# Optimization experiments

Measured on AMD Instinct MI355X. Metric: run time of the kernel, lower is better.

The kernel has to match this reference:

```python
import jax, jax.numpy as jnp
import numpy as np

B, T, D, H = 512, 256, 64, 128


def _uniform(key, shape, stdv):
    return jax.random.uniform(key, shape, jnp.float32, -stdv, stdv)


def setup_inputs() -> dict:
    key = jax.random.key(0)
    ks = jax.random.split(key, 20)
    x_t = jax.random.normal(ks[0], (B, T, D), jnp.float32)
    masks = (jax.random.uniform(ks[1], (B, T, D)) < 0.8).astype(jnp.float32)
    deltas = jax.random.uniform(ks[2], (B, T, D), jnp.float32)
    sH = 1.0 / np.sqrt(H)
    sD = 1.0 / np.sqrt(D)
    return {
        "x_t": x_t, "masks": masks, "deltas": deltas,
        # TemporalDecay h: [H, D]
        "Wdh": _uniform(ks[3], (H, D), sH), "bdh": _uniform(ks[4], (H,), sH),
        # TemporalDecay x (diag): [D, D]
        "Wdx": _uniform(ks[5], (D, D), sD), "bdx": _uniform(ks[6], (D,), sD),
        # hist_reg Linear(H -> D)
        "Whr": _uniform(ks[7], (D, H), sH), "bhr": _uniform(ks[8], (D,), sH),
        "Wfr": _uniform(ks[9], (D, D), sD), "bfr": _uniform(ks[10], (D,), sD),
        # weight_combine Linear(2D -> D)
        "Wwc": _uniform(ks[11], (D, 2 * D), 1.0 / np.sqrt(2 * D)),
        "bwc": _uniform(ks[12], (D,), 1.0 / np.sqrt(2 * D)),
        # LSTMCell(2D -> H)
        "W_ih": _uniform(ks[13], (4 * H, 2 * D), sH), "W_hh": _uniform(ks[14], (4 * H, H), sH),
        "b_ih": _uniform(ks[15], (4 * H,), sH), "b_hh": _uniform(ks[16], (4 * H,), sH),
    }


def reference(x_t, masks, deltas, Wdh, bdh, Wdx, bdx, Whr, bhr, Wfr, bfr, Wwc, bwc, W_ih, W_hh, b_ih, b_hh):
    Bv, Tv, Dv = x_t.shape
    Hv = Wdh.shape[0]
    eye = jnp.eye(Dv, dtype=x_t.dtype)
    Wdx_m = Wdx * eye              # diagonal temporal decay
    Wfr_m = Wfr * (1.0 - eye)

    def step(carry, xs):
        h, c, loss = carry
        x, m, d = xs
        gamma_h = jnp.exp(-jax.nn.relu(d @ Wdh.T + bdh))   # [B,H]
        gamma_x = jnp.exp(-jax.nn.relu(d @ Wdx_m.T + bdx))  # [B,D]
        h = h * gamma_h
        x_h = h @ Whr.T + bhr
        msum = jnp.sum(m) + 1e-5
        loss = loss + jnp.sum(jnp.abs(x - x_h) * m) / msum
        x_c = m * x + (1.0 - m) * x_h
        z_h = x_c @ Wfr_m.T + bfr
        loss = loss + jnp.sum(jnp.abs(x - z_h) * m) / msum
        alpha = jnp.concatenate([gamma_x, m], axis=1) @ Wwc.T + bwc
        c_h = alpha * z_h + (1.0 - alpha) * x_h
        loss = loss + jnp.sum(jnp.abs(x - c_h) * m) / msum
        c_c = m * x + (1.0 - m) * c_h
        inp = jnp.concatenate([c_c, m], axis=1)            # [B,2D]
        gates = inp @ W_ih.T + b_ih + h @ W_hh.T + b_hh    # [B,4H]
        i, f, g, o = jnp.split(gates, 4, axis=1)
        c = jax.nn.sigmoid(f) * c + jax.nn.sigmoid(i) * jnp.tanh(g)
        h = jax.nn.sigmoid(o) * jnp.tanh(c)
        return (h, c, loss), c_c

    h0 = jnp.zeros((Bv, Hv), x_t.dtype)
    c0 = jnp.zeros((Bv, Hv), x_t.dtype)
    xs = (jnp.swapaxes(x_t, 0, 1), jnp.swapaxes(masks, 0, 1), jnp.swapaxes(deltas, 0, 1))
    (h, c, loss), imps = jax.lax.scan(step, (h0, c0, jnp.float32(0.0)), xs)
    imputations = jnp.swapaxes(imps, 0, 1)                 # [B,T,D]
    return loss / Tv, imputations
```

## Files before the change

### kernel.cpp

```cpp
#include <hip/hip_runtime.h>
#include <hip/hip_bf16.h>

typedef __bf16 bf16x8 __attribute__((ext_vector_type(8)));
typedef float f32x4 __attribute__((ext_vector_type(4)));

#define NB 512
#define NT 256
#define ND 64
#define NH 128
#define PART_IDX 256
#define FLAG_IDX 320

__device__ __forceinline__ float bf2f(__hip_bfloat16 v){ return __bfloat162float(v); }
__device__ __forceinline__ __hip_bfloat16 f2bf(float v){ return __float2bfloat16(v); }

__device__ __forceinline__ float ldF(const float* p){ return *p; }
__device__ __forceinline__ float ldF(const __hip_bfloat16* p){ return __bfloat162float(*p); }
__device__ __forceinline__ void  stF(float* p, float v){ *p = v; }
__device__ __forceinline__ void  stF(__hip_bfloat16* p, float v){ *p = __float2bfloat16(v); }

__device__ __forceinline__ void ld2(const float* p, float& a, float& b){
    float2 v = *reinterpret_cast<const float2*>(p); a = v.x; b = v.y;
}
__device__ __forceinline__ void ld2(const __hip_bfloat16* p, float& a, float& b){
    unsigned u = *reinterpret_cast<const unsigned*>(p);
    unsigned short s0 = (unsigned short)(u & 0xffffu), s1 = (unsigned short)(u >> 16);
    a = __bfloat162float(*reinterpret_cast<__hip_bfloat16*>(&s0));
    b = __bfloat162float(*reinterpret_cast<__hip_bfloat16*>(&s1));
}

__device__ __forceinline__ bf16x8 ldfrag(const __hip_bfloat16* p){
    return *reinterpret_cast<const bf16x8*>(p);
}
__device__ __forceinline__ bf16x8 ldfrag(const float* p){
    f32x4 a = *reinterpret_cast<const f32x4*>(p);
    f32x4 b = *reinterpret_cast<const f32x4*>(p + 4);
    bf16x8 r;
    #pragma unroll
    for (int i = 0; i < 4; ++i){
        __hip_bfloat16 ha = __float2bfloat16(a[i]);
        __hip_bfloat16 hb = __float2bfloat16(b[i]);
        r[i]   = *reinterpret_cast<__bf16*>(&ha);
        r[4+i] = *reinterpret_cast<__bf16*>(&hb);
    }
    return r;
}
__device__ __forceinline__ bf16x8 ldbf8(const __hip_bfloat16* p){
    return *reinterpret_cast<const bf16x8*>(p);
}

template<typename T> __device__ __forceinline__ float wantFlag(){ return sizeof(T)==4 ? 1.f : 0.f; }

__device__ __forceinline__ f32x4 mfma16(bf16x8 a, bf16x8 b, f32x4 c){
    return __builtin_amdgcn_mfma_f32_16x16x32_bf16(a, b, c, 0, 0, 0);
}
__device__ __forceinline__ float fsig(float x){ return 1.f/(1.f+__expf(-x)); }
__device__ __forceinline__ float ftanh(float x){ return 1.f - 2.f/(__expf(2.f*x)+1.f); }

__global__ void detect_kernel(const void* __restrict__ x, float* __restrict__ WS){
    if (threadIdx.x == 0 && blockIdx.x == 0){
        const unsigned short* u = (const unsigned short*)x;
        int weird = 0;
        for (int i = 0; i < 256; ++i){
            unsigned e = (u[i] >> 7) & 0xFF;
            if (e == 0xFF || e >= 0x8A || (e != 0 && e <= 0x5A)) ++weird;
        }
        WS[FLAG_IDX] = (weird >= 16) ? 1.f : 0.f;
    }
}

template<typename T>
__global__ __launch_bounds__(256) void msum_kernel(const T* __restrict__ M,
                                                   float* __restrict__ WS){
    if (WS[FLAG_IDX] != wantFlag<T>()) return;
    int t = blockIdx.x;
    int tid = threadIdx.x;
    int col = tid & 63;
    int bg  = tid >> 6;
    float s = 0.f;
    for (int b = bg; b < NB; b += 4)
        s += ldF(&M[((size_t)b*NT + t)*ND + col]);
    #pragma unroll
    for (int off = 32; off > 0; off >>= 1) s += __shfl_down(s, off);
    __shared__ float r4[4];
    if ((tid & 63) == 0) r4[bg] = s;
    __syncthreads();
    if (tid == 0) WS[t] = 1.f / (r4[0] + r4[1] + r4[2] + r4[3] + 1e-5f);
}

template<typename T>
__global__ __launch_bounds__(512, 2) void brits_main(
    const T* __restrict__ X,  const T* __restrict__ M,
    const T* __restrict__ DL,
    const T* __restrict__ Wdh, const T* __restrict__ bdh,
    const T* __restrict__ Wdx, const T* __restrict__ bdx,
    const T* __restrict__ Whr, const T* __restrict__ bhr,
    const T* __restrict__ Wfr, const T* __restrict__ bfr,
    const T* __restrict__ Wwc, const T* __restrict__ bwc,
    const T* __restrict__ Wih, const T* __restrict__ Whh,
    const T* __restrict__ bih, const T* __restrict__ bhh,
    T* __restrict__ OUT, float* __restrict__ WS)
{
    if (WS[FLAG_IDX] != wantFlag<T>()) return;

    __shared__ __align__(16) __hip_bfloat16 sAg[16][264];
    __shared__ __align__(16) __hip_bfloat16 sAal[16][136];
    __shared__ __align__(16) __hip_bfloat16 sXc[16][72];
    __shared__ __align__(16) __hip_bfloat16 sDL[16][72];
    __shared__ float sX [16][68];
    __shared__ float sXh[16][68];
    __shared__ float sZh[16][68];
    __shared__ float sAl[16][68];
    __shared__ float sRed[8];

    const int tid = threadIdx.x;
    const int w  = tid >> 6;
    const int l  = tid & 63;
    const int lr = l & 15;
    const int lg = l >> 4;
    const int b0 = blockIdx.x * 16;

    const int hcol = 16*w + lr;
    const float bdh_r = ldF(&bdh[hcol]);
    const float gb_i = ldF(&bih[hcol])      + ldF(&bhh[hcol]);
    const float gb_f = ldF(&bih[NH+hcol])   + ldF(&bhh[NH+hcol]);
    const float gb_g = ldF(&bih[2*NH+hcol]) + ldF(&bhh[2*NH+hcol]);
    const float gb_o = ldF(&bih[3*NH+hcol]) + ldF(&bhh[3*NH+hcol]);

    bf16x8 pB0 = ldfrag(Wdh + (size_t)hcol*ND + lg*8);
    bf16x8 pB1 = ldfrag(Wdh + (size_t)hcol*ND + 32 + lg*8);
    bf16x8 qB0 = {}, qB1 = {}, qB2 = {}, qB3 = {}, rB0 = {}, rB1 = {};
    float b1_r = 0.f, b2_r = 0.f, b3_r = 0.f;
    int dcol;
    if (w < 4){
        dcol = 16*w + lr;
        b1_r = ldF(&bhr[dcol]);  b2_r = ldF(&bfr[dcol]);
        qB0 = ldfrag(Whr + (size_t)dcol*NH + lg*8);
        qB1 = ldfrag(Whr + (size_t)dcol*NH + 32 + lg*8);
        qB2 = ldfrag(Whr + (size_t)dcol*NH + 64 + lg*8);
        qB3 = ldfrag(Whr + (size_t)dcol*NH + 96 + lg*8);
        rB0 = ldfrag(Wfr + (size_t)dcol*ND + lg*8);
        rB1 = ldfrag(Wfr + (size_t)dcol*ND + 32 + lg*8);
        int kb0 = lg*8;      if (dcol >= kb0 && dcol < kb0+8) rB0[dcol-kb0] = (__bf16)0.f;
        int kb1 = 32 + lg*8; if (dcol >= kb1 && dcol < kb1+8) rB1[dcol-kb1] = (__bf16)0.f;
    } else {
        dcol = 16*(w-4) + lr;
        b3_r = ldF(&bwc[dcol]);
        qB0 = ldfrag(Wwc + (size_t)dcol*2*ND + lg*8);
        qB1 = ldfrag(Wwc + (size_t)dcol*2*ND + 32 + lg*8);
        qB2 = ldfrag(Wwc + (size_t)dcol*2*ND + 64 + lg*8);
        qB3 = ldfrag(Wwc + (size_t)dcol*2*ND + 96 + lg*8);
    }

    const int r0 = tid >> 5;
    const int c0 = (tid & 31) * 2;
    const float wdg0 = ldF(&Wdx[(size_t)c0*ND + c0]);
    const float wdg1 = ldF(&Wdx[(size_t)(c0+1)*ND + (c0+1)]);
    const float bdx0 = ldF(&bdx[c0]);
    const float bdx1 = ldF(&bdx[c0+1]);

    float hreg[4] = {0.f,0.f,0.f,0.f};
    float creg[4] = {0.f,0.f,0.f,0.f};
    float lacc = 0.f;

    float pd0, pd1, pm0, pm1, px0, px1;

    {
        size_t g0 = ((size_t)(b0+r0)*NT + 0)*ND + c0;
        ld2(DL + g0, pd0, pd1);
        ld2(M  + g0, pm0, pm1);
        ld2(X  + g0, px0, px1);
        sDL[r0][c0]   = f2bf(pd0);
        sDL[r0][c0+1] = f2bf(pd1);
        #pragma unroll
        for (int r = 0; r < 4; ++r) sAg[lg*4+r][128 + hcol] = f2bf(0.f);
    }
    float inv_cur = WS[0];
    __syncthreads();

    #pragma unroll 1
    for (int t = 0; t < NT; ++t){
        const float inv_ms = inv_cur;
        {
            f32x4 acc = {0.f,0.f,0.f,0.f};
            acc = mfma16(ldbf8(&sDL[lr][0  + lg*8]), pB0, acc);
            acc = mfma16(ldbf8(&sDL[lr][32 + lg*8]), pB1, acc);
            #pragma unroll
            for (int r = 0; r < 4; ++r){
                float gm = __expf(-fmaxf(acc[r] + bdh_r, 0.f));
                hreg[r] *= gm;
                sAg[lg*4+r][128 + hcol] = f2bf(hreg[r]);
            }
            float gx0 = __expf(-fmaxf(pd0*wdg0 + bdx0, 0.f));
            float gx1 = __expf(-fmaxf(pd1*wdg1 + bdx1, 0.f));
            sAal[r0][c0]      = f2bf(gx0);
            sAal[r0][c0+1]    = f2bf(gx1);
            sAal[r0][64+c0]   = f2bf(pm0);
            sAal[r0][64+c0+1] = f2bf(pm1);
            sAg[r0][64+c0]    = f2bf(pm0);
            sAg[r0][64+c0+1]  = f2bf(pm1);
            sX[r0][c0]   = px0;
            sX[r0][c0+1] = px1;
        }
        __syncthreads();
        if (w < 4){
            f32x4 acc = {0.f,0.f,0.f,0.f};
            acc = mfma16(ldbf8(&sAg[lr][128 + 0  + lg*8]), qB0, acc);
            acc = mfma16(ldbf8(&sAg[lr][128 + 32 + lg*8]), qB1, acc);
            acc = mfma16(ldbf8(&sAg[lr][128 + 64 + lg*8]), qB2, acc);
            acc = mfma16(ldbf8(&sAg[lr][128 + 96 + lg*8]), qB3, acc);
            #pragma unroll
            for (int r = 0; r < 4; ++r){
                int row = lg*4 + r;
                float xh = acc[r] + b1_r;
                sXh[row][dcol] = xh;
                float mv = bf2f(sAg[row][64+dcol]);
                float xv = sX[row][dcol];
                float xc = mv*xv + (1.f-mv)*xh;
                sXc[row][dcol] = f2bf(xc);
                lacc += fabsf(xv - xh) * mv * inv_ms;
            }
        } else {
            f32x4 acc = {0.f,0.f,0.f,0.f};
            acc = mfma16(ldbf8(&sAal[lr][0  + lg*8]), qB0, acc);
            acc = mfma16(ldbf8(&sAal[lr][32 + lg*8]), qB1, acc);
            acc = mfma16(ldbf8(&sAal[lr][64 + lg*8]), qB2, acc);
            acc = mfma16(ldbf8(&sAal[lr][96 + lg*8]), qB3, acc);
            #pragma unroll
            for (int r = 0; r < 4; ++r) sAl[lg*4+r][dcol] = acc[r] + b3_r;
        }
        __syncthreads();
        if (w < 4){
            f32x4 acc = {0.f,0.f,0.f,0.f};
            acc = mfma16(ldbf8(&sXc[lr][0  + lg*8]), rB0, acc);
            acc = mfma16(ldbf8(&sXc[lr][32 + lg*8]), rB1, acc);
            #pragma unroll
            for (int r = 0; r < 4; ++r) sZh[lg*4+r][dcol] = acc[r] + b2_r;
        }
        __syncthreads();
        {
            size_t g = ((size_t)(b0+r0)*NT + t)*ND + c0;
            #pragma unroll
            for (int e = 0; e < 2; ++e){
                int col = c0 + e;
                float xv = sX[r0][col];
                float mv = bf2f(sAg[r0][64+col]);
                float zh = sZh[r0][col];
                float xh = sXh[r0][col];
                float al = sAl[r0][col];
                float ch = al*zh + (1.f-al)*xh;
                lacc += (fabsf(xv - zh) + fabsf(xv - ch)) * mv * inv_ms;
                float cc = mv*xv + (1.f-mv)*ch;
                stF(&OUT[1 + g + e], cc);
                sAg[r0][col] = f2bf(cc);
            }
        }
        __syncthreads();
        {
            const int tn = (t+1 < NT) ? t+1 : t;
            size_t gE = ((size_t)(b0+r0)*NT + tn)*ND + c0;
            ld2(DL + gE, pd0, pd1);
            ld2(M  + gE, pm0, pm1);
            ld2(X  + gE, px0, px1);
            float inv_next = WS[tn];

            bf16x8 af[8];
            #pragma unroll
            for (int kk = 0; kk < 8; ++kk) af[kk] = ldbf8(&sAg[lr][kk*32 + lg*8]);
            const T* wih_b = Wih + (size_t)hcol*128;
            const T* whh_b = Whh + (size_t)hcol*128;
            f32x4 gacc[4];
            #pragma unroll
            for (int g = 0; g < 4; ++g){
                const T* wr = wih_b + (size_t)g*NH*128;
                const T* hr = whh_b + (size_t)g*NH*128;
                f32x4 a = {0.f,0.f,0.f,0.f};
                a = mfma16(af[0], ldfrag(wr + 0  + lg*8), a);
                a = mfma16(af[1], ldfrag(wr + 32 + lg*8), a);
                a = mfma16(af[2], ldfrag(wr + 64 + lg*8), a);
                a = mfma16(af[3], ldfrag(wr + 96 + lg*8), a);
                a = mfma16(af[4], ldfrag(hr + 0  + lg*8), a);
                a = mfma16(af[5], ldfrag(hr + 32 + lg*8), a);
                a = mfma16(af[6], ldfrag(hr + 64 + lg*8), a);
                a = mfma16(af[7], ldfrag(hr + 96 + lg*8), a);
                gacc[g] = a;
            }
            #pragma unroll
            for (int r = 0; r < 4; ++r){
                float iv = fsig(gacc[0][r] + gb_i);
                float fv = fsig(gacc[1][r] + gb_f);
                float gv = ftanh(gacc[2][r] + gb_g);
                float ov = fsig(gacc[3][r] + gb_o);
                creg[r] = fv*creg[r] + iv*gv;
                hreg[r] = ov*ftanh(creg[r]);
            }
            sDL[r0][c0]   = f2bf(pd0);
            sDL[r0][c0+1] = f2bf(pd1);
            inv_cur = inv_next;
        }
        __syncthreads();
    }

    #pragma unroll
    for (int off = 32; off > 0; off >>= 1) lacc += __shfl_down(lacc, off);
    if (l == 0) sRed[w] = lacc;
    __syncthreads();
    if (tid == 0){
        float s = 0.f;
        #pragma unroll
        for (int i = 0; i < 8; ++i) s += sRed[i];
        WS[PART_IDX + blockIdx.x] = s;
    }
}

template<typename T>
__global__ void fin_kernel(const float* __restrict__ WS, T* __restrict__ OUT){
    if (WS[FLAG_IDX] != wantFlag<T>()) return;
    if (threadIdx.x == 0 && blockIdx.x == 0){
        float s = 0.f;
        for (int i = 0; i < 32; ++i) s += WS[PART_IDX + i];
        stF(&OUT[0], s / (float)NT);
    }
}

template<typename T>
static void launch_all(void* const* d_in, void* d_out, float* WS, hipStream_t stream){
    const T* X   = (const T*)d_in[0];
    const T* M   = (const T*)d_in[1];
    const T* DL  = (const T*)d_in[2];
    const T* Wdh = (const T*)d_in[3];
    const T* bdh = (const T*)d_in[4];
    const T* Wdx = (const T*)d_in[5];
    const T* bdx = (const T*)d_in[6];
    const T* Whr = (const T*)d_in[7];
    const T* bhr = (const T*)d_in[8];
    const T* Wfr = (const T*)d_in[9];
    const T* bfr = (const T*)d_in[10];
    const T* Wwc = (const T*)d_in[11];
    const T* bwc = (const T*)d_in[12];
    const T* Wih = (const T*)d_in[13];
    const T* Whh = (const T*)d_in[14];
    const T* bih = (const T*)d_in[15];
    const T* bhh = (const T*)d_in[16];
    T* OUT = (T*)d_out;
    msum_kernel<T><<<dim3(NT), dim3(256), 0, stream>>>(M, WS);
    brits_main<T><<<dim3(32), dim3(512), 0, stream>>>(X, M, DL, Wdh, bdh, Wdx, bdx,
                                                      Whr, bhr, Wfr, bfr, Wwc, bwc,
                                                      Wih, Whh, bih, bhh, OUT, WS);
    fin_kernel<T><<<dim3(1), dim3(64), 0, stream>>>(WS, OUT);
}

extern "C" void kernel_launch(void* const* d_in, const int* in_sizes, int n_in,
                              void* d_out, int out_size, void* d_ws, size_t ws_size,
                              hipStream_t stream) {
    float* WS = (float*)d_ws;
    detect_kernel<<<dim3(1), dim3(64), 0, stream>>>(d_in[0], WS);
    launch_all<__hip_bfloat16>(d_in, d_out, WS, stream);
    launch_all<float>(d_in, d_out, WS, stream);
}
```

Baseline: 805.3 us.

## Fold decay phase into LSTM phase and double-buffer h/mask to drop a barrier

Moves the gamma_h decay GEMM (loading deltas for the next step straight from global memory into MFMA fragments) and the gamma_x/mask/x staging into the tail of the previous step's LSTM phase. The separate first phase and its __syncthreads are removed from each timestep. h and mask are double-buffered in shared memory and the concatenated LSTM input buffer is split into separate arrays. This removes one barrier per step and shortens the serial chain, at the cost of extra global loads and MFMAs in the LSTM phase. It also stores only the decayed h rather than keeping h in registers.

```diff
diff --git a/kernel.cpp b/kernel.cpp
--- a/kernel.cpp
+++ b/kernel.cpp
@@ -48,6 +48,33 @@
 __device__ __forceinline__ bf16x8 ldbf8(const __hip_bfloat16* p){
     return *reinterpret_cast<const bf16x8*>(p);
 }
+
+template<typename T> struct PF;
+template<> struct PF<float>{
+    f32x4 a, b;
+    __device__ __forceinline__ void load(const float* p){
+        a = *reinterpret_cast<const f32x4*>(p);
+        b = *reinterpret_cast<const f32x4*>(p + 4);
+    }
+    __device__ __forceinline__ bf16x8 get() const {
+        bf16x8 r;
+        #pragma unroll
+        for (int i = 0; i < 4; ++i){
+            __hip_bfloat16 ha = __float2bfloat16(a[i]);
+            __hip_bfloat16 hb = __float2bfloat16(b[i]);
+            r[i]   = *reinterpret_cast<const __bf16*>(&ha);
+            r[4+i] = *reinterpret_cast<const __bf16*>(&hb);
+        }
+        return r;
+    }
+};
+template<> struct PF<__hip_bfloat16>{
+    bf16x8 a;
+    __device__ __forceinline__ void load(const __hip_bfloat16* p){
+        a = *reinterpret_cast<const bf16x8*>(p);
+    }
+    __device__ __forceinline__ bf16x8 get() const { return a; }
+};
 
 template<typename T> __device__ __forceinline__ float wantFlag(){ return sizeof(T)==4 ? 1.f : 0.f; }
 
@@ -103,10 +130,11 @@
 {
     if (WS[FLAG_IDX] != wantFlag<T>()) return;
 
-    __shared__ __align__(16) __hip_bfloat16 sAg[16][264];
-    __shared__ __align__(16) __hip_bfloat16 sAal[16][136];
+    __shared__ __align__(16) __hip_bfloat16 sH [2][16][136];
+    __shared__ __align__(16) __hip_bfloat16 sM [2][16][72];
+    __shared__ __align__(16) __hip_bfloat16 sGX[16][72];
+    __shared__ __align__(16) __hip_bfloat16 sCC[16][72];
     __shared__ __align__(16) __hip_bfloat16 sXc[16][72];
-    __shared__ __align__(16) __hip_bfloat16 sDL[16][72];
     __shared__ float sX [16][68];
     __shared__ float sXh[16][68];
     __shared__ float sZh[16][68];
@@ -159,21 +187,22 @@
     const float bdx0 = ldF(&bdx[c0]);
     const float bdx1 = ldF(&bdx[c0+1]);
 
-    float hreg[4] = {0.f,0.f,0.f,0.f};
     float creg[4] = {0.f,0.f,0.f,0.f};
     float lacc = 0.f;
-
     float pd0, pd1, pm0, pm1, px0, px1;
 
     {
         size_t g0 = ((size_t)(b0+r0)*NT + 0)*ND + c0;
-        ld2(DL + g0, pd0, pd1);
-        ld2(M  + g0, pm0, pm1);
-        ld2(X  + g0, px0, px1);
-        sDL[r0][c0]   = f2bf(pd0);
-        sDL[r0][c0+1] = f2bf(pd1);
+        float d0, d1, m0, m1, x0, x1;
+        ld2(DL + g0, d0, d1); ld2(M + g0, m0, m1); ld2(X + g0, x0, x1);
+        sGX[r0][c0]    = f2bf(__expf(-fmaxf(d0*wdg0 + bdx0, 0.f)));
+        sGX[r0][c0+1]  = f2bf(__expf(-fmaxf(d1*wdg1 + bdx1, 0.f)));
+        sM[0][r0][c0]   = f2bf(m0);
+        sM[0][r0][c0+1] = f2bf(m1);
+        sX[r0][c0]   = x0;
+        sX[r0][c0+1] = x1;
         #pragma unroll
-        for (int r = 0; r < 4; ++r) sAg[lg*4+r][128 + hcol] = f2bf(0.f);
+        for (int r = 0; r < 4; ++r) sH[0][lg*4+r][hcol] = f2bf(0.f);
     }
     float inv_cur = WS[0];
     __syncthreads();
@@ -181,40 +210,19 @@
     #pragma unroll 1
     for (int t = 0; t < NT; ++t){
         const float inv_ms = inv_cur;
-        {
-            f32x4 acc = {0.f,0.f,0.f,0.f};
-            acc = mfma16(ldbf8(&sDL[lr][0  + lg*8]), pB0, acc);
-            acc = mfma16(ldbf8(&sDL[lr][32 + lg*8]), pB1, acc);
-            #pragma unroll
-            for (int r = 0; r < 4; ++r){
-                float gm = __expf(-fmaxf(acc[r] + bdh_r, 0.f));
-                hreg[r] *= gm;
-                sAg[lg*4+r][128 + hcol] = f2bf(hreg[r]);
-            }
-            float gx0 = __expf(-fmaxf(pd0*wdg0 + bdx0, 0.f));
-            float gx1 = __expf(-fmaxf(pd1*wdg1 + bdx1, 0.f));
-            sAal[r0][c0]      = f2bf(gx0);
-            sAal[r0][c0+1]    = f2bf(gx1);
-            sAal[r0][64+c0]   = f2bf(pm0);
-            sAal[r0][64+c0+1] = f2bf(pm1);
-            sAg[r0][64+c0]    = f2bf(pm0);
-            sAg[r0][64+c0+1]  = f2bf(pm1);
-            sX[r0][c0]   = px0;
-            sX[r0][c0+1] = px1;
-        }
-        __syncthreads();
+        const int cur = t & 1, nxt = cur ^ 1;
         if (w < 4){
             f32x4 acc = {0.f,0.f,0.f,0.f};
-            acc = mfma16(ldbf8(&sAg[lr][128 + 0  + lg*8]), qB0, acc);
-            acc = mfma16(ldbf8(&sAg[lr][128 + 32 + lg*8]), qB1, acc);
-            acc = mfma16(ldbf8(&sAg[lr][128 + 64 + lg*8]), qB2, acc);
-            acc = mfma16(ldbf8(&sAg[lr][128 + 96 + lg*8]), qB3, acc);
+            acc = mfma16(ldbf8(&sH[cur][lr][0  + lg*8]), qB0, acc);
+            acc = mfma16(ldbf8(&sH[cur][lr][32 + lg*8]), qB1, acc);
+            acc = mfma16(ldbf8(&sH[cur][lr][64 + lg*8]), qB2, acc);
+            acc = mfma16(ldbf8(&sH[cur][lr][96 + lg*8]), qB3, acc);
             #pragma unroll
             for (int r = 0; r < 4; ++r){
                 int row = lg*4 + r;
                 float xh = acc[r] + b1_r;
                 sXh[row][dcol] = xh;
-                float mv = bf2f(sAg[row][64+dcol]);
+                float mv = bf2f(sM[cur][row][dcol]);
                 float xv = sX[row][dcol];
                 float xc = mv*xv + (1.f-mv)*xh;
                 sXc[row][dcol] = f2bf(xc);
@@ -222,10 +230,10 @@
             }
         } else {
             f32x4 acc = {0.f,0.f,0.f,0.f};
-            acc = mfma16(ldbf8(&sAal[lr][0  + lg*8]), qB0, acc);
-            acc = mfma16(ldbf8(&sAal[lr][32 + lg*8]), qB1, acc);
-            acc = mfma16(ldbf8(&sAal[lr][64 + lg*8]), qB2, acc);
-            acc = mfma16(ldbf8(&sAal[lr][96 + lg*8]), qB3, acc);
+            acc = mfma16(ldbf8(&sGX[lr][0  + lg*8]),      qB0, acc);
+            acc = mfma16(ldbf8(&sGX[lr][32 + lg*8]),      qB1, acc);
+            acc = mfma16(ldbf8(&sM[cur][lr][0  + lg*8]),  qB2, acc);
+            acc = mfma16(ldbf8(&sM[cur][lr][32 + lg*8]),  qB3, acc);
             #pragma unroll
             for (int r = 0; r < 4; ++r) sAl[lg*4+r][dcol] = acc[r] + b3_r;
         }
@@ -244,7 +252,7 @@
             for (int e = 0; e < 2; ++e){
                 int col = c0 + e;
                 float xv = sX[r0][col];
-                float mv = bf2f(sAg[r0][64+col]);
+                float mv = bf2f(sM[cur][r0][col]);
                 float zh = sZh[r0][col];
                 float xh = sXh[r0][col];
                 float al = sAl[r0][col];
@@ -252,12 +260,16 @@
                 lacc += (fabsf(xv - zh) + fabsf(xv - ch)) * mv * inv_ms;
                 float cc = mv*xv + (1.f-mv)*ch;
                 stF(&OUT[1 + g + e], cc);
-                sAg[r0][col] = f2bf(cc);
+                sCC[r0][col] = f2bf(cc);
             }
         }
         __syncthreads();
         {
             const int tn = (t+1 < NT) ? t+1 : t;
+            PF<T> pfA0, pfA1;
+            const T* drow = DL + ((size_t)(b0+lr)*NT + tn)*ND;
+            pfA0.load(drow + lg*8);
+            pfA1.load(drow + 32 + lg*8);
             size_t gE = ((size_t)(b0+r0)*NT + tn)*ND + c0;
             ld2(DL + gE, pd0, pd1);
             ld2(M  + gE, pm0, pm1);
@@ -265,8 +277,14 @@
             float inv_next = WS[tn];
 
             bf16x8 af[8];
-            #pragma unroll
-            for (int kk = 0; kk < 8; ++kk) af[kk] = ldbf8(&sAg[lr][kk*32 + lg*8]);
+            af[0] = ldbf8(&sCC[lr][0  + lg*8]);
+            af[1] = ldbf8(&sCC[lr][32 + lg*8]);
+            af[2] = ldbf8(&sM[cur][lr][0  + lg*8]);
+            af[3] = ldbf8(&sM[cur][lr][32 + lg*8]);
+            af[4] = ldbf8(&sH[cur][lr][0  + lg*8]);
+            af[5] = ldbf8(&sH[cur][lr][32 + lg*8]);
+            af[6] = ldbf8(&sH[cur][lr][64 + lg*8]);
+            af[7] = ldbf8(&sH[cur][lr][96 + lg*8]);
             const T* wih_b = Wih + (size_t)hcol*128;
             const T* whh_b = Whh + (size_t)hcol*128;
             f32x4 gacc[4];
@@ -285,6 +303,9 @@
                 a = mfma16(af[7], ldfrag(hr + 96 + lg*8), a);
                 gacc[g] = a;
             }
+            f32x4 ga = {0.f,0.f,0.f,0.f};
+            ga = mfma16(pfA0.get(), pB0, ga);
+            ga = mfma16(pfA1.get(), pB1, ga);
             #pragma unroll
             for (int r = 0; r < 4; ++r){
                 float iv = fsig(gacc[0][r] + gb_i);
@@ -292,10 +313,16 @@
                 float gv = ftanh(gacc[2][r] + gb_g);
                 float ov = fsig(gacc[3][r] + gb_o);
                 creg[r] = fv*creg[r] + iv*gv;
-                hreg[r] = ov*ftanh(creg[r]);
+                float hn = ov*ftanh(creg[r]);
+                float gh = __expf(-fmaxf(ga[r] + bdh_r, 0.f));
+                sH[nxt][lg*4+r][hcol] = f2bf(hn * gh);
             }
-            sDL[r0][c0]   = f2bf(pd0);
-            sDL[r0][c0+1] = f2bf(pd1);
+            sGX[r0][c0]     = f2bf(__expf(-fmaxf(pd0*wdg0 + bdx0, 0.f)));
+            sGX[r0][c0+1]   = f2bf(__expf(-fmaxf(pd1*wdg1 + bdx1, 0.f)));
+            sM[nxt][r0][c0]   = f2bf(pm0);
+            sM[nxt][r0][c0+1] = f2bf(pm1);
+            sX[r0][c0]   = px0;
+            sX[r0][c0+1] = px1;
             inv_cur = inv_next;
         }
         __syncthreads();
```

Result: slower. 1.320 ms (+63.9%).
